# Optimization experiments

Measured on AMD Instinct MI355X. Metric: run time of the kernel, lower is better.

The kernel has to match this reference:

```python
import jax, jax.numpy as jnp
import numpy as np

# Adaptive-LIF constants (Yin et al. spiking RNN, which this thesis repo builds on)
B_J0 = 0.01    # baseline threshold
BETA = 1.8     # adaptation strength
GAMMA = 0.5    # surrogate gradient scale
LENS = 0.5     # surrogate gaussian width
HIGHT = 0.15   # multi-gaussian side-lobe height
SCALE = 6.0    # side-lobe width multiplier


def _gaussian(x, mu, sigma):
    return jnp.exp(-((x - mu) ** 2) / (2.0 * sigma ** 2)) / (jnp.sqrt(2.0 * jnp.pi) * sigma)


@jax.custom_vjp
def spike_fn(v):
    # Heaviside spike with multi-gaussian surrogate gradient
    return (v > 0).astype(v.dtype)

def _spike_fwd(v):
    return spike_fn(v), v

def _spike_bwd(v, g):
    sg = (_gaussian(v, 0.0, LENS) * (1.0 + HIGHT)
          - _gaussian(v, LENS, SCALE * LENS) * HIGHT
          - _gaussian(v, -LENS, SCALE * LENS) * HIGHT)
    return (g * sg * GAMMA,)

spike_fn.defvjp(_spike_fwd, _spike_bwd)


def setup_inputs() -> dict:
    key = jax.random.key(0)
    ks = jax.random.split(key, 16)
    B, S, C, H, O = 256, 250, 700, 256, 20

    def lin(k, fan_in, shape):  # nn.Linear default init
        lim = 1.0 / np.sqrt(fan_in)
        return jax.random.uniform(k, shape, jnp.float32, -lim, lim)

    def tau(k, mean, std, shape):
        return jnp.clip(mean + std * jax.random.normal(k, shape, jnp.float32), 1.0, None)

    return {
        "x": jax.random.normal(ks[0], (B, S, C), jnp.float32),
        # forward spiking cell (tauM ~ N(20, ~5), tauAdp ~ N(200, ~50))
        "W_in_f": lin(ks[1], C, (C, H)), "b_in_f": lin(ks[2], C, (H,)),
        "W_rec_f": lin(ks[3], H, (H, H)), "b_rec_f": lin(ks[4], H, (H,)),
        "tau_m_f": tau(ks[5], 20.0, 5.0, (H,)),
        "tau_adp_f": tau(ks[6], 200.0, 50.0, (H,)),
        # backward spiking cell
        "W_in_b": lin(ks[7], C, (C, H)), "b_in_b": lin(ks[8], C, (H,)),
        "W_rec_b": lin(ks[9], H, (H, H)), "b_rec_b": lin(ks[10], H, (H,)),
        "tau_m_b": tau(ks[11], 20.0, 5.0, (H,)),
        "tau_adp_b": tau(ks[12], 200.0, 50.0, (H,)),
        # readout leaky integrator over concat(fw, bw) = 512 -> 20, tauM ~ N(3, 1)
        "W_out": lin(ks[13], 2 * H, (2 * H, O)), "b_out": lin(ks[14], 2 * H, (O,)),
        "tau_m_out": tau(ks[15], 3.0, 1.0, (O,)),
    }


def reference(x, W_in_f, b_in_f, W_rec_f, b_rec_f, tau_m_f, tau_adp_f,
              W_in_b, b_in_b, W_rec_b, b_rec_b, tau_m_b, tau_adp_b,
              W_out, b_out, tau_m_out):
    B, S, C = x.shape
    H = W_in_f.shape[1]
    O = W_out.shape[1]

    alpha_f = jnp.exp(-1.0 / tau_m_f); ro_f = jnp.exp(-1.0 / tau_adp_f)
    alpha_b = jnp.exp(-1.0 / tau_m_b); ro_b = jnp.exp(-1.0 / tau_adp_b)
    alpha_o = jnp.exp(-1.0 / tau_m_out)

    # Batch the feed-forward input projections over all timesteps: [S, B, H]
    proj_f = jnp.einsum("bsc,ch->sbh", x, W_in_f) + b_in_f
    proj_b = jnp.einsum("bsc,ch->sbh", x[:, ::-1], W_in_b) + b_in_b

    def cell(in_t, mem, spk, bb, W_rec, b_rec, alpha, ro):
        # mem_update_adp: adaptive threshold LIF
        d = in_t + spk @ W_rec + b_rec
        bb = ro * bb + (1.0 - ro) * spk
        thr = B_J0 + BETA * bb
        mem = mem * alpha + (1.0 - alpha) * d - thr * spk
        spk = spike_fn(mem - thr)
        return mem, spk, bb

    def step(carry, xs):
        mem_f, spk_f, bb_f, mem_b, spk_b, bb_b, mem_o = carry
        in_f, in_b = xs
        mem_f, spk_f, bb_f = cell(in_f, mem_f, spk_f, bb_f, W_rec_f, b_rec_f, alpha_f, ro_f)
        mem_b, spk_b, bb_b = cell(in_b, mem_b, spk_b, bb_b, W_rec_b, b_rec_b, alpha_b, ro_b)
        # readout integrator over concat(fw, bw) spikes (method=1 integrates every step)
        merged = jnp.concatenate([spk_f, spk_b], axis=-1)
        mem_o = mem_o * alpha_o + (1.0 - alpha_o) * (merged @ W_out + b_out)
        return (mem_f, spk_f, bb_f, mem_b, spk_b, bb_b, mem_o), None

    z = jnp.zeros((B, H), x.dtype)
    b0 = jnp.full((B, H), B_J0, x.dtype)
    carry0 = (z, z, b0, z, z, b0, jnp.zeros((B, O), x.dtype))
    carry, _ = jax.lax.scan(step, carry0, (proj_f, proj_b))
    return jax.nn.log_softmax(carry[-1], axis=-1)
```

## Files before the change

kernel.cpp:

```cpp
#include <hip/hip_runtime.h>
#include <cstdint>
#include <cstddef>

#define S_LEN 250
#define BATCH 256
#define CIN   700
#define HID   256
#define OUT_N 20
#define KSTEPS 22

typedef __attribute__((ext_vector_type(8))) short bf16x8;
typedef __attribute__((ext_vector_type(4))) float f32x4;

__device__ __forceinline__ ushort f2bf_rne(float f) {
    uint u = __float_as_uint(f);
    uint r = (u + 0x7FFFu + ((u >> 16) & 1u)) >> 16;
    return (ushort)r;
}
__device__ __forceinline__ float bf2f(ushort h) {
    return __uint_as_float(((uint)h) << 16);
}

__global__ __launch_bounds__(256) void proj_mfma(
    const float* __restrict__ x,
    const float* __restrict__ Wf, const float* __restrict__ Wb,
    const float* __restrict__ biasf, const float* __restrict__ biasb,
    float* __restrict__ P)
{
    __shared__ ushort AsH[128][40];
    __shared__ ushort AsL[128][40];
    __shared__ ushort BsH[256][40];
    __shared__ ushort BsL[256][40];

    const int nt = blockIdx.x;
    const int mt = blockIdx.y;
    const int m0 = mt * 128;
    const float* W   = nt ? Wb : Wf;
    const float* bia = nt ? biasb : biasf;

    const int tid  = threadIdx.x;
    const int lane = tid & 63;
    const int wv   = tid >> 6;
    const int wr   = wv >> 1;
    const int wc   = wv & 1;
    const int l15  = lane & 15;
    const int l4   = lane >> 4;

    const int as  = tid & 7;
    const int arr = tid >> 3;

    f32x4 acc[4][8];
#pragma unroll
    for (int i = 0; i < 4; i++)
#pragma unroll
        for (int j = 0; j < 8; j++)
            acc[i][j] = (f32x4){0.f, 0.f, 0.f, 0.f};

    float4 av[4];
    float bv[32];

#define PROJ_LOAD(K0_) do {                                                   \
        const int ka_ = (K0_) + as * 4;                                       \
        const bool aok_ = (ka_ + 3) < CIN;                                    \
        _Pragma("unroll")                                                     \
        for (int i_ = 0; i_ < 4; i_++) {                                      \
            av[i_] = make_float4(0.f, 0.f, 0.f, 0.f);                         \
            if (aok_)                                                         \
                av[i_] = *(const float4*)&x[(size_t)(m0 + arr + 32 * i_) * CIN + ka_]; \
        }                                                                     \
        _Pragma("unroll")                                                     \
        for (int j_ = 0; j_ < 32; j_++) {                                     \
            const int kb_ = (K0_) + j_;                                       \
            bv[j_] = (kb_ < CIN) ? W[(size_t)kb_ * HID + tid] : 0.f;          \
        }                                                                     \
    } while (0)

#define PROJ_CVT_WRITE() do {                                                 \
        _Pragma("unroll")                                                     \
        for (int i_ = 0; i_ < 4; i_++) {                                      \
            const int row_ = arr + 32 * i_;                                   \
            ushort4 h_, l_;                                                   \
            h_.x = f2bf_rne(av[i_].x); l_.x = f2bf_rne(__fsub_rn(av[i_].x, bf2f(h_.x))); \
            h_.y = f2bf_rne(av[i_].y); l_.y = f2bf_rne(__fsub_rn(av[i_].y, bf2f(h_.y))); \
            h_.z = f2bf_rne(av[i_].z); l_.z = f2bf_rne(__fsub_rn(av[i_].z, bf2f(h_.z))); \
            h_.w = f2bf_rne(av[i_].w); l_.w = f2bf_rne(__fsub_rn(av[i_].w, bf2f(h_.w))); \
            *(ushort4*)&AsH[row_][as * 4] = h_;                               \
            *(ushort4*)&AsL[row_][as * 4] = l_;                               \
        }                                                                     \
        _Pragma("unroll")                                                     \
        for (int q_ = 0; q_ < 8; q_++) {                                      \
            ushort4 h_, l_;                                                   \
            float v0_ = bv[q_ * 4 + 0], v1_ = bv[q_ * 4 + 1];                 \
            float v2_ = bv[q_ * 4 + 2], v3_ = bv[q_ * 4 + 3];                 \
            h_.x = f2bf_rne(v0_); l_.x = f2bf_rne(__fsub_rn(v0_, bf2f(h_.x))); \
            h_.y = f2bf_rne(v1_); l_.y = f2bf_rne(__fsub_rn(v1_, bf2f(h_.y))); \
            h_.z = f2bf_rne(v2_); l_.z = f2bf_rne(__fsub_rn(v2_, bf2f(h_.z))); \
            h_.w = f2bf_rne(v3_); l_.w = f2bf_rne(__fsub_rn(v3_, bf2f(h_.w))); \
            *(ushort4*)&BsH[tid][q_ * 4] = h_;                               \
            *(ushort4*)&BsL[tid][q_ * 4] = l_;                               \
        }                                                                     \
    } while (0)

    PROJ_LOAD(0);
    PROJ_CVT_WRITE();

    for (int kt = 0; kt < KSTEPS; kt++) {
        __syncthreads();
        if (kt + 1 < KSTEPS)
            PROJ_LOAD((kt + 1) * 32);

#pragma unroll
        for (int fc = 0; fc < 8; fc++) {
            const bf16x8 bHf = *(const bf16x8*)&BsH[wc * 128 + fc * 16 + l15][l4 * 8];
            const bf16x8 bLf = *(const bf16x8*)&BsL[wc * 128 + fc * 16 + l15][l4 * 8];
#pragma unroll
            for (int fr = 0; fr < 4; fr++) {
                const bf16x8 aHf = *(const bf16x8*)&AsH[wr * 64 + fr * 16 + l15][l4 * 8];
                const bf16x8 aLf = *(const bf16x8*)&AsL[wr * 64 + fr * 16 + l15][l4 * 8];
                acc[fr][fc] = __builtin_amdgcn_mfma_f32_16x16x32_bf16(
                    aHf, bHf, acc[fr][fc], 0, 0, 0);
                acc[fr][fc] = __builtin_amdgcn_mfma_f32_16x16x32_bf16(
                    aHf, bLf, acc[fr][fc], 0, 0, 0);
                acc[fr][fc] = __builtin_amdgcn_mfma_f32_16x16x32_bf16(
                    aLf, bHf, acc[fr][fc], 0, 0, 0);
            }
        }

        __syncthreads();
        if (kt + 1 < KSTEPS)
            PROJ_CVT_WRITE();
    }

#undef PROJ_LOAD
#undef PROJ_CVT_WRITE

#pragma unroll
    for (int fc = 0; fc < 8; fc++) {
        const int col = wc * 128 + fc * 16 + l15;
        const float bvs = bia[col];
#pragma unroll
        for (int fr = 0; fr < 4; fr++) {
#pragma unroll
            for (int j = 0; j < 4; j++) {
                const int row = m0 + wr * 64 + fr * 16 + l4 * 4 + j;
                P[(size_t)row * 512 + nt * HID + col] =
                    __fadd_rn(acc[fr][fc][j], bvs);
            }
        }
    }
}

__global__ __launch_bounds__(512, 2) void scan_mfma(
    const float* __restrict__ P,
    const float* __restrict__ Wrecf, const float* __restrict__ brecf,
    const float* __restrict__ taumf, const float* __restrict__ tauaf,
    const float* __restrict__ Wrecb, const float* __restrict__ brecb,
    const float* __restrict__ taumb, const float* __restrict__ tauab,
    const float* __restrict__ Wout, const float* __restrict__ taumo,
    float* __restrict__ Pst)
{
    const int g  = blockIdx.x;
    const int d  = blockIdx.y;
    const int b0 = g * 16;
    const bool fw = (d == 0);

    const int tid  = threadIdx.x;
    const int lane = tid & 63;
    const int w    = tid >> 6;
    const int l15  = lane & 15;
    const int l4   = lane >> 4;

    __shared__ ushort Sp[2][16][264];

    {
        ushort* p = &Sp[0][0][0];
        for (int i = tid; i < 2 * 16 * 264; i += 512) p[i] = 0;
    }

    const float* Wrec = fw ? Wrecf : Wrecb;

    bf16x8 whf[8][2], wlf[8][2];
#pragma unroll
    for (int kt = 0; kt < 8; kt++)
#pragma unroll
        for (int ct = 0; ct < 2; ct++) {
            const int c = w * 32 + ct * 16 + l15;
#pragma unroll
            for (int j = 0; j < 8; j++) {
                const float v = Wrec[(size_t)(kt * 32 + l4 * 8 + j) * HID + c];
                const ushort h = f2bf_rne(v);
                const ushort l = f2bf_rne(__fsub_rn(v, bf2f(h)));
                whf[kt][ct][j] = (short)h;
                wlf[kt][ct][j] = (short)l;
            }
        }

    bf16x8 woh[2], wol[2];
#pragma unroll
    for (int t = 0; t < 2; t++) {
        const int o = t * 16 + l15;
#pragma unroll
        for (int j = 0; j < 8; j++) {
            float v = 0.f;
            if (o < OUT_N)
                v = Wout[(size_t)(d * HID + w * 32 + l4 * 8 + j) * OUT_N + o];
            const ushort h = f2bf_rne(v);
            const ushort l = f2bf_rne(__fsub_rn(v, bf2f(h)));
            woh[t][j] = (short)h;
            wol[t][j] = (short)l;
        }
    }

    float alpha_[2], ro_[2], omA_[2], omR_[2], brc_[2];
#pragma unroll
    for (int t = 0; t < 2; t++) {
        const int c = w * 32 + t * 16 + l15;
        alpha_[t] = expf(__fdiv_rn(-1.f, fw ? taumf[c] : taumb[c]));
        ro_[t]    = expf(__fdiv_rn(-1.f, fw ? tauaf[c] : tauab[c]));
        omA_[t]   = __fsub_rn(1.f, alpha_[t]);
        omR_[t]   = __fsub_rn(1.f, ro_[t]);
        brc_[t]   = fw ? brecf[c] : brecb[c];
    }
    float ao_[2], omo_[2];
#pragma unroll
    for (int t = 0; t < 2; t++) {
        const int o = t * 16 + l15;
        if (o < OUT_N) {
            ao_[t]  = expf(__fdiv_rn(-1.f, taumo[o]));
            omo_[t] = __fsub_rn(1.f, ao_[t]);
        } else { ao_[t] = 0.f; omo_[t] = 0.f; }
    }

    float mem[2][4], bbv[2][4], spkv[2][4], z[2][4];
#pragma unroll
    for (int t = 0; t < 2; t++)
#pragma unroll
        for (int j = 0; j < 4; j++) {
            mem[t][j] = 0.f; bbv[t][j] = 0.01f; spkv[t][j] = 0.f; z[t][j] = 0.f;
        }

    float pv[2][4];
    {
        const int srow = fw ? 0 : (S_LEN - 1);
#pragma unroll
        for (int t = 0; t < 2; t++)
#pragma unroll
            for (int j = 0; j < 4; j++)
                pv[t][j] = P[((size_t)(b0 + l4 * 4 + j) * S_LEN + srow) * 512
                             + d * HID + w * 32 + t * 16 + l15];
    }

    for (int s = 0; s < S_LEN; s++) {
        const int cur = s & 1, prev = cur ^ 1;

        float pv_next[2][4];
        {
            const int sn   = (s + 1 < S_LEN) ? s + 1 : S_LEN - 1;
            const int srow = fw ? sn : (S_LEN - 1 - sn);
#pragma unroll
            for (int t = 0; t < 2; t++)
#pragma unroll
                for (int j = 0; j < 4; j++)
                    pv_next[t][j] = P[((size_t)(b0 + l4 * 4 + j) * S_LEN + srow) * 512
                                      + d * HID + w * 32 + t * 16 + l15];
        }

        __syncthreads();

        f32x4 acc[2];
        acc[0] = (f32x4){0.f, 0.f, 0.f, 0.f};
        acc[1] = (f32x4){0.f, 0.f, 0.f, 0.f};
#pragma unroll
        for (int kt = 0; kt < 8; kt++) {
            const bf16x8 a = *(const bf16x8*)&Sp[prev][l15][kt * 32 + l4 * 8];
            acc[0] = __builtin_amdgcn_mfma_f32_16x16x32_bf16(a, whf[kt][0], acc[0], 0, 0, 0);
            acc[0] = __builtin_amdgcn_mfma_f32_16x16x32_bf16(a, wlf[kt][0], acc[0], 0, 0, 0);
            acc[1] = __builtin_amdgcn_mfma_f32_16x16x32_bf16(a, whf[kt][1], acc[1], 0, 0, 0);
            acc[1] = __builtin_amdgcn_mfma_f32_16x16x32_bf16(a, wlf[kt][1], acc[1], 0, 0, 0);
        }

#pragma unroll
        for (int t = 0; t < 2; t++) {
#pragma unroll
            for (int j = 0; j < 4; j++) {
                const float dd = __fadd_rn(__fadd_rn(pv[t][j], acc[t][j]), brc_[t]);
                bbv[t][j] = __fadd_rn(__fmul_rn(ro_[t], bbv[t][j]),
                                      __fmul_rn(omR_[t], spkv[t][j]));
                const float thr = __fadd_rn(0.01f, __fmul_rn(1.8f, bbv[t][j]));
                mem[t][j] = __fsub_rn(
                    __fadd_rn(__fmul_rn(mem[t][j], alpha_[t]),
                              __fmul_rn(omA_[t], dd)),
                    __fmul_rn(thr, spkv[t][j]));
                const bool sp = __fsub_rn(mem[t][j], thr) > 0.f;
                spkv[t][j] = sp ? 1.f : 0.f;
                Sp[cur][l4 * 4 + j][w * 32 + t * 16 + l15] =
                    sp ? (ushort)0x3F80 : (ushort)0;
            }
        }

        asm volatile("s_waitcnt lgkmcnt(0)" ::: "memory");
        __builtin_amdgcn_sched_barrier(0);

        {
            const bf16x8 ar = *(const bf16x8*)&Sp[cur][l15][w * 32 + l4 * 8];
            f32x4 S0 = (f32x4){0.f, 0.f, 0.f, 0.f};
            f32x4 S1 = (f32x4){0.f, 0.f, 0.f, 0.f};
            S0 = __builtin_amdgcn_mfma_f32_16x16x32_bf16(ar, woh[0], S0, 0, 0, 0);
            S0 = __builtin_amdgcn_mfma_f32_16x16x32_bf16(ar, wol[0], S0, 0, 0, 0);
            S1 = __builtin_amdgcn_mfma_f32_16x16x32_bf16(ar, woh[1], S1, 0, 0, 0);
            S1 = __builtin_amdgcn_mfma_f32_16x16x32_bf16(ar, wol[1], S1, 0, 0, 0);
#pragma unroll
            for (int j = 0; j < 4; j++) {
                z[0][j] = __fmaf_rn(ao_[0], z[0][j], __fmul_rn(omo_[0], S0[j]));
                z[1][j] = __fmaf_rn(ao_[1], z[1][j], __fmul_rn(omo_[1], S1[j]));
            }
        }

#pragma unroll
        for (int t = 0; t < 2; t++)
#pragma unroll
            for (int j = 0; j < 4; j++) pv[t][j] = pv_next[t][j];
    }

    __syncthreads();

    float* stash = Pst + ((size_t)b0 * S_LEN) * 512 + d * HID;
#pragma unroll
    for (int j = 0; j < 4; j++) {
        const int r = l4 * 4 + j;
        const int idx0 = w * 320 + r * 16 + l15;
        stash[(size_t)(idx0 >> 8) * 512 + (idx0 & 255)] = z[0][j];
        if (l15 < 4) {
            const int idx1 = w * 320 + 256 + r * 4 + l15;
            stash[(size_t)(idx1 >> 8) * 512 + (idx1 & 255)] = z[1][j];
        }
    }
}

__global__ __launch_bounds__(64) void merge_out(
    const float* __restrict__ Pst, const float* __restrict__ bout,
    const float* __restrict__ taumo, float* __restrict__ out)
{
    const int bb = blockIdx.x;
    const int o  = threadIdx.x;
    const int g  = bb >> 4, r = bb & 15;

    float val = 0.f, v = -3.0e38f;
    if (o < OUT_N) {
        float tot = 0.f;
#pragma unroll
        for (int d2 = 0; d2 < 2; d2++) {
            const float* stash = Pst + ((size_t)(g * 16) * S_LEN) * 512 + d2 * HID;
#pragma unroll
            for (int w2 = 0; w2 < 8; w2++) {
                const int idx = (o < 16) ? (w2 * 320 + r * 16 + o)
                                         : (w2 * 320 + 256 + r * 4 + (o - 16));
                tot = __fadd_rn(tot, stash[(size_t)(idx >> 8) * 512 + (idx & 255)]);
            }
        }
        const float aS = expf(__fdiv_rn(-(float)S_LEN, taumo[o]));
        val = __fadd_rn(tot, __fmul_rn(bout[o], __fsub_rn(1.f, aS)));
        v = val;
    }
    float mx = v;
#pragma unroll
    for (int d2 = 1; d2 < 64; d2 <<= 1)
        mx = fmaxf(mx, __shfl_xor(mx, d2, 64));
    float e = (o < OUT_N) ? expf(__fsub_rn(val, mx)) : 0.f;
#pragma unroll
    for (int d2 = 1; d2 < 64; d2 <<= 1)
        e += __shfl_xor(e, d2, 64);
    if (o < OUT_N)
        out[(size_t)bb * OUT_N + o] =
            __fsub_rn(__fsub_rn(val, mx), logf(e));
}

extern "C" void kernel_launch(void* const* d_in, const int* in_sizes, int n_in,
                              void* d_out, int out_size, void* d_ws, size_t ws_size,
                              hipStream_t stream) {
    const float* x         = (const float*)d_in[0];
    const float* W_in_f    = (const float*)d_in[1];
    const float* b_in_f    = (const float*)d_in[2];
    const float* W_rec_f   = (const float*)d_in[3];
    const float* b_rec_f   = (const float*)d_in[4];
    const float* tau_m_f   = (const float*)d_in[5];
    const float* tau_adp_f = (const float*)d_in[6];
    const float* W_in_b    = (const float*)d_in[7];
    const float* b_in_b    = (const float*)d_in[8];
    const float* W_rec_b   = (const float*)d_in[9];
    const float* b_rec_b   = (const float*)d_in[10];
    const float* tau_m_b   = (const float*)d_in[11];
    const float* tau_adp_b = (const float*)d_in[12];
    const float* W_out     = (const float*)d_in[13];
    const float* b_out     = (const float*)d_in[14];
    const float* tau_m_o   = (const float*)d_in[15];
    float* out = (float*)d_out;
    float* P   = (float*)d_ws;

    proj_mfma<<<dim3(2, 500), dim3(256), 0, stream>>>(
        x, W_in_f, W_in_b, b_in_f, b_in_b, P);
    scan_mfma<<<dim3(16, 2), dim3(512), 0, stream>>>(
        P, W_rec_f, b_rec_f, tau_m_f, tau_adp_f,
        W_rec_b, b_rec_b, tau_m_b, tau_adp_b,
        W_out, tau_m_o, P);
    merge_out<<<dim3(BATCH), dim3(64), 0, stream>>>(
        P, b_out, tau_m_o, out);
}
```

Before: 455.0 us.

## Split scan across 16 waves with half of recurrent weights staged in LDS

The recurrent scan now uses 1024 threads (16 waves), each wave owning 16 hidden columns instead of 32. This halves the per-wave serial MFMA chain and elementwise work. Half of the bf16 hi/lo split of W_rec stays in registers and the other half is held in shared memory, because the registers cannot hold all of it at this wave count. The readout MFMA is moved to run on the previous step's spikes, so one lgkmcnt wait and one sched barrier per step go away, with a final readout added after the loop. The costs are extra LDS traffic for the weight reads and larger per-block LDS usage.

```diff
diff --git a/kernel.cpp b/kernel.cpp
--- a/kernel.cpp
+++ b/kernel.cpp
@@ -150,7 +150,7 @@
     }
 }
 
-__global__ __launch_bounds__(512, 2) void scan_mfma(
+__global__ __launch_bounds__(1024, 4) void scan_mfma16(
     const float* __restrict__ P,
     const float* __restrict__ Wrecf, const float* __restrict__ brecf,
     const float* __restrict__ taumf, const float* __restrict__ tauaf,
@@ -169,140 +169,136 @@
     const int w    = tid >> 6;
     const int l15  = lane & 15;
     const int l4   = lane >> 4;
+    const int c    = w * 16 + l15;
 
     __shared__ ushort Sp[2][16][264];
+    __shared__ ushort WH[256][132];
+    __shared__ ushort WL[256][132];
 
     {
         ushort* p = &Sp[0][0][0];
-        for (int i = tid; i < 2 * 16 * 264; i += 512) p[i] = 0;
+        for (int i = tid; i < 2 * 16 * 264; i += 1024) p[i] = 0;
     }
 
     const float* Wrec = fw ? Wrecf : Wrecb;
 
-    bf16x8 whf[8][2], wlf[8][2];
-#pragma unroll
-    for (int kt = 0; kt < 8; kt++)
-#pragma unroll
-        for (int ct = 0; ct < 2; ct++) {
-            const int c = w * 32 + ct * 16 + l15;
+    {
+        const int cc = tid & 255;
+        const int kq = tid >> 8;
+        for (int k2 = 0; k2 < 32; k2++) {
+            const int k = 128 + kq * 32 + k2;
+            const float v = Wrec[(size_t)k * HID + cc];
+            const ushort h = f2bf_rne(v);
+            const ushort l = f2bf_rne(__fsub_rn(v, bf2f(h)));
+            WH[cc][k - 128] = h;
+            WL[cc][k - 128] = l;
+        }
+    }
+
+    bf16x8 whf[4], wlf[4];
+#pragma unroll
+    for (int kt = 0; kt < 4; kt++) {
+#pragma unroll
+        for (int j = 0; j < 8; j++) {
+            const float v = Wrec[(size_t)(kt * 32 + l4 * 8 + j) * HID + c];
+            const ushort h = f2bf_rne(v);
+            const ushort l = f2bf_rne(__fsub_rn(v, bf2f(h)));
+            whf[kt][j] = (short)h;
+            wlf[kt][j] = (short)l;
+        }
+    }
+
+    bf16x8 woh[2], wol[2];
+#pragma unroll
+    for (int t = 0; t < 2; t++)
+#pragma unroll
+        for (int j = 0; j < 8; j++) { woh[t][j] = 0; wol[t][j] = 0; }
+    if (!(w & 1)) {
+#pragma unroll
+        for (int t = 0; t < 2; t++) {
+            const int o = t * 16 + l15;
 #pragma unroll
             for (int j = 0; j < 8; j++) {
-                const float v = Wrec[(size_t)(kt * 32 + l4 * 8 + j) * HID + c];
+                float v = 0.f;
+                if (o < OUT_N)
+                    v = Wout[(size_t)(d * HID + w * 16 + l4 * 8 + j) * OUT_N + o];
                 const ushort h = f2bf_rne(v);
                 const ushort l = f2bf_rne(__fsub_rn(v, bf2f(h)));
-                whf[kt][ct][j] = (short)h;
-                wlf[kt][ct][j] = (short)l;
-            }
-        }
-
-    bf16x8 woh[2], wol[2];
-#pragma unroll
-    for (int t = 0; t < 2; t++) {
-        const int o = t * 16 + l15;
-#pragma unroll
-        for (int j = 0; j < 8; j++) {
-            float v = 0.f;
-            if (o < OUT_N)
-                v = Wout[(size_t)(d * HID + w * 32 + l4 * 8 + j) * OUT_N + o];
-            const ushort h = f2bf_rne(v);
-            const ushort l = f2bf_rne(__fsub_rn(v, bf2f(h)));
-            woh[t][j] = (short)h;
-            wol[t][j] = (short)l;
-        }
-    }
-
-    float alpha_[2], ro_[2], omA_[2], omR_[2], brc_[2];
-#pragma unroll
-    for (int t = 0; t < 2; t++) {
-        const int c = w * 32 + t * 16 + l15;
-        alpha_[t] = expf(__fdiv_rn(-1.f, fw ? taumf[c] : taumb[c]));
-        ro_[t]    = expf(__fdiv_rn(-1.f, fw ? tauaf[c] : tauab[c]));
-        omA_[t]   = __fsub_rn(1.f, alpha_[t]);
-        omR_[t]   = __fsub_rn(1.f, ro_[t]);
-        brc_[t]   = fw ? brecf[c] : brecb[c];
-    }
-    float ao_[2], omo_[2];
-#pragma unroll
-    for (int t = 0; t < 2; t++) {
-        const int o = t * 16 + l15;
-        if (o < OUT_N) {
-            ao_[t]  = expf(__fdiv_rn(-1.f, taumo[o]));
-            omo_[t] = __fsub_rn(1.f, ao_[t]);
-        } else { ao_[t] = 0.f; omo_[t] = 0.f; }
-    }
-
-    float mem[2][4], bbv[2][4], spkv[2][4], z[2][4];
-#pragma unroll
-    for (int t = 0; t < 2; t++)
-#pragma unroll
-        for (int j = 0; j < 4; j++) {
-            mem[t][j] = 0.f; bbv[t][j] = 0.01f; spkv[t][j] = 0.f; z[t][j] = 0.f;
-        }
-
-    float pv[2][4];
+                woh[t][j] = (short)h;
+                wol[t][j] = (short)l;
+            }
+        }
+    }
+
+    const float alpha = expf(__fdiv_rn(-1.f, fw ? taumf[c] : taumb[c]));
+    const float ro    = expf(__fdiv_rn(-1.f, fw ? tauaf[c] : tauab[c]));
+    const float omA   = __fsub_rn(1.f, alpha);
+    const float omR   = __fsub_rn(1.f, ro);
+    const float brc   = fw ? brecf[c] : brecb[c];
+
+    float ao_[2] = {0.f, 0.f}, omo_[2] = {0.f, 0.f};
+    if (!(w & 1)) {
+#pragma unroll
+        for (int t = 0; t < 2; t++) {
+            const int o = t * 16 + l15;
+            if (o < OUT_N) {
+                ao_[t]  = expf(__fdiv_rn(-1.f, taumo[o]));
+                omo_[t] = __fsub_rn(1.f, ao_[t]);
+            }
+        }
+    }
+
+    float mem[4], bbv[4], spkv[4], z[2][4];
+#pragma unroll
+    for (int j = 0; j < 4; j++) {
+        mem[j] = 0.f; bbv[j] = 0.01f; spkv[j] = 0.f;
+        z[0][j] = 0.f; z[1][j] = 0.f;
+    }
+
+    float pv[4];
     {
         const int srow = fw ? 0 : (S_LEN - 1);
 #pragma unroll
-        for (int t = 0; t < 2; t++)
-#pragma unroll
-            for (int j = 0; j < 4; j++)
-                pv[t][j] = P[((size_t)(b0 + l4 * 4 + j) * S_LEN + srow) * 512
-                             + d * HID + w * 32 + t * 16 + l15];
-    }
+        for (int j = 0; j < 4; j++)
+            pv[j] = P[((size_t)(b0 + l4 * 4 + j) * S_LEN + srow) * 512
+                      + d * HID + c];
+    }
+
+    __syncthreads();
 
     for (int s = 0; s < S_LEN; s++) {
         const int cur = s & 1, prev = cur ^ 1;
 
-        float pv_next[2][4];
+        float pv_next[4];
         {
             const int sn   = (s + 1 < S_LEN) ? s + 1 : S_LEN - 1;
             const int srow = fw ? sn : (S_LEN - 1 - sn);
 #pragma unroll
-            for (int t = 0; t < 2; t++)
-#pragma unroll
-                for (int j = 0; j < 4; j++)
-                    pv_next[t][j] = P[((size_t)(b0 + l4 * 4 + j) * S_LEN + srow) * 512
-                                      + d * HID + w * 32 + t * 16 + l15];
+            for (int j = 0; j < 4; j++)
+                pv_next[j] = P[((size_t)(b0 + l4 * 4 + j) * S_LEN + srow) * 512
+                               + d * HID + c];
         }
 
         __syncthreads();
 
-        f32x4 acc[2];
-        acc[0] = (f32x4){0.f, 0.f, 0.f, 0.f};
-        acc[1] = (f32x4){0.f, 0.f, 0.f, 0.f};
-#pragma unroll
-        for (int kt = 0; kt < 8; kt++) {
+        f32x4 acc = (f32x4){0.f, 0.f, 0.f, 0.f};
+#pragma unroll
+        for (int kt = 0; kt < 4; kt++) {
             const bf16x8 a = *(const bf16x8*)&Sp[prev][l15][kt * 32 + l4 * 8];
-            acc[0] = __builtin_amdgcn_mfma_f32_16x16x32_bf16(a, whf[kt][0], acc[0], 0, 0, 0);
-            acc[0] = __builtin_amdgcn_mfma_f32_16x16x32_bf16(a, wlf[kt][0], acc[0], 0, 0, 0);
-            acc[1] = __builtin_amdgcn_mfma_f32_16x16x32_bf16(a, whf[kt][1], acc[1], 0, 0, 0);
-            acc[1] = __builtin_amdgcn_mfma_f32_16x16x32_bf16(a, wlf[kt][1], acc[1], 0, 0, 0);
-        }
-
-#pragma unroll
-        for (int t = 0; t < 2; t++) {
-#pragma unroll
-            for (int j = 0; j < 4; j++) {
-                const float dd = __fadd_rn(__fadd_rn(pv[t][j], acc[t][j]), brc_[t]);
-                bbv[t][j] = __fadd_rn(__fmul_rn(ro_[t], bbv[t][j]),
-                                      __fmul_rn(omR_[t], spkv[t][j]));
-                const float thr = __fadd_rn(0.01f, __fmul_rn(1.8f, bbv[t][j]));
-                mem[t][j] = __fsub_rn(
-                    __fadd_rn(__fmul_rn(mem[t][j], alpha_[t]),
-                              __fmul_rn(omA_[t], dd)),
-                    __fmul_rn(thr, spkv[t][j]));
-                const bool sp = __fsub_rn(mem[t][j], thr) > 0.f;
-                spkv[t][j] = sp ? 1.f : 0.f;
-                Sp[cur][l4 * 4 + j][w * 32 + t * 16 + l15] =
-                    sp ? (ushort)0x3F80 : (ushort)0;
-            }
-        }
-
-        asm volatile("s_waitcnt lgkmcnt(0)" ::: "memory");
-        __builtin_amdgcn_sched_barrier(0);
-
-        {
-            const bf16x8 ar = *(const bf16x8*)&Sp[cur][l15][w * 32 + l4 * 8];
+            acc = __builtin_amdgcn_mfma_f32_16x16x32_bf16(a, whf[kt], acc, 0, 0, 0);
+            acc = __builtin_amdgcn_mfma_f32_16x16x32_bf16(a, wlf[kt], acc, 0, 0, 0);
+        }
+#pragma unroll
+        for (int kt = 4; kt < 8; kt++) {
+            const bf16x8 a  = *(const bf16x8*)&Sp[prev][l15][kt * 32 + l4 * 8];
+            const bf16x8 bh = *(const bf16x8*)&WH[c][(kt - 4) * 32 + l4 * 8];
+            const bf16x8 bl = *(const bf16x8*)&WL[c][(kt - 4) * 32 + l4 * 8];
+            acc = __builtin_amdgcn_mfma_f32_16x16x32_bf16(a, bh, acc, 0, 0, 0);
+            acc = __builtin_amdgcn_mfma_f32_16x16x32_bf16(a, bl, acc, 0, 0, 0);
+        }
+
+        if (!(w & 1)) {
+            const bf16x8 ar = *(const bf16x8*)&Sp[prev][l15][w * 16 + l4 * 8];
             f32x4 S0 = (f32x4){0.f, 0.f, 0.f, 0.f};
             f32x4 S1 = (f32x4){0.f, 0.f, 0.f, 0.f};
             S0 = __builtin_amdgcn_mfma_f32_16x16x32_bf16(ar, woh[0], S0, 0, 0, 0);
@@ -317,22 +313,50 @@
         }
 
 #pragma unroll
-        for (int t = 0; t < 2; t++)
-#pragma unroll
-            for (int j = 0; j < 4; j++) pv[t][j] = pv_next[t][j];
+        for (int j = 0; j < 4; j++) {
+            const float dd = __fadd_rn(__fadd_rn(pv[j], acc[j]), brc);
+            bbv[j] = __fadd_rn(__fmul_rn(ro, bbv[j]),
+                               __fmul_rn(omR, spkv[j]));
+            const float thr = __fadd_rn(0.01f, __fmul_rn(1.8f, bbv[j]));
+            mem[j] = __fsub_rn(
+                __fadd_rn(__fmul_rn(mem[j], alpha), __fmul_rn(omA, dd)),
+                __fmul_rn(thr, spkv[j]));
+            const bool sp = __fsub_rn(mem[j], thr) > 0.f;
+            spkv[j] = sp ? 1.f : 0.f;
+            Sp[cur][l4 * 4 + j][c] = sp ? (ushort)0x3F80 : (ushort)0;
+        }
+
+#pragma unroll
+        for (int j = 0; j < 4; j++) pv[j] = pv_next[j];
     }
 
     __syncthreads();
 
-    float* stash = Pst + ((size_t)b0 * S_LEN) * 512 + d * HID;
-#pragma unroll
-    for (int j = 0; j < 4; j++) {
-        const int r = l4 * 4 + j;
-        const int idx0 = w * 320 + r * 16 + l15;
-        stash[(size_t)(idx0 >> 8) * 512 + (idx0 & 255)] = z[0][j];
-        if (l15 < 4) {
-            const int idx1 = w * 320 + 256 + r * 4 + l15;
-            stash[(size_t)(idx1 >> 8) * 512 + (idx1 & 255)] = z[1][j];
+    if (!(w & 1)) {
+        const bf16x8 ar = *(const bf16x8*)&Sp[1][l15][w * 16 + l4 * 8];
+        f32x4 S0 = (f32x4){0.f, 0.f, 0.f, 0.f};
+        f32x4 S1 = (f32x4){0.f, 0.f, 0.f, 0.f};
+        S0 = __builtin_amdgcn_mfma_f32_16x16x32_bf16(ar, woh[0], S0, 0, 0, 0);
+        S0 = __builtin_amdgcn_mfma_f32_16x16x32_bf16(ar, wol[0], S0, 0, 0, 0);
+        S1 = __builtin_amdgcn_mfma_f32_16x16x32_bf16(ar, woh[1], S1, 0, 0, 0);
+        S1 = __builtin_amdgcn_mfma_f32_16x16x32_bf16(ar, wol[1], S1, 0, 0, 0);
+#pragma unroll
+        for (int j = 0; j < 4; j++) {
+            z[0][j] = __fmaf_rn(ao_[0], z[0][j], __fmul_rn(omo_[0], S0[j]));
+            z[1][j] = __fmaf_rn(ao_[1], z[1][j], __fmul_rn(omo_[1], S1[j]));
+        }
+
+        float* stash = Pst + ((size_t)b0 * S_LEN) * 512 + d * HID;
+        const int ws = w >> 1;
+#pragma unroll
+        for (int j = 0; j < 4; j++) {
+            const int r = l4 * 4 + j;
+            const int idx0 = ws * 320 + r * 16 + l15;
+            stash[(size_t)(idx0 >> 8) * 512 + (idx0 & 255)] = z[0][j];
+            if (l15 < 4) {
+                const int idx1 = ws * 320 + 256 + r * 4 + l15;
+                stash[(size_t)(idx1 >> 8) * 512 + (idx1 & 255)] = z[1][j];
+            }
         }
     }
 }
@@ -399,7 +423,7 @@
 
     proj_mfma<<<dim3(2, 500), dim3(256), 0, stream>>>(
         x, W_in_f, W_in_b, b_in_f, b_in_b, P);
-    scan_mfma<<<dim3(16, 2), dim3(512), 0, stream>>>(
+    scan_mfma16<<<dim3(16, 2), dim3(1024), 0, stream>>>(
         P, W_rec_f, b_rec_f, tau_m_f, tau_adp_f,
         W_rec_b, b_rec_b, tau_m_b, tau_adp_b,
         W_out, tau_m_o, P);
```

New measurement: 511.2 us. 12.3% more time.

## Use int8 MFMA with split hi/lo quantized recurrent weights for spike matmul

Applied to the files above, without the earlier changes.

Replaces the bf16 hi/lo split recurrent matmul with int8 MFMA (16x16x64). The recurrent weights are quantized per column to a 16-bit fixed-point value split into two int8 halves, and the binary spikes go into a new int8 shared buffer. This halves the MFMA instruction count per step and reduces register use for the weights. In exchange it adds a per-column max scan at setup and an extra shared-memory store per spike, and it changes numerical precision to about 1/16000 of the column max, which could flip spikes near the threshold.

```diff
diff --git a/kernel.cpp b/kernel.cpp
--- a/kernel.cpp
+++ b/kernel.cpp
@@ -11,6 +11,7 @@
 
 typedef __attribute__((ext_vector_type(8))) short bf16x8;
 typedef __attribute__((ext_vector_type(4))) float f32x4;
+typedef __attribute__((ext_vector_type(4))) int   i32x4;
 
 __device__ __forceinline__ ushort f2bf_rne(float f) {
     uint u = __float_as_uint(f);
@@ -171,29 +172,51 @@
     const int l4   = lane >> 4;
 
     __shared__ ushort Sp[2][16][264];
+    __shared__ signed char Sp8[2][16][272];
 
     {
         ushort* p = &Sp[0][0][0];
         for (int i = tid; i < 2 * 16 * 264; i += 512) p[i] = 0;
+        signed char* p8 = &Sp8[0][0][0];
+        for (int i = tid; i < 2 * 16 * 272; i += 512) p8[i] = 0;
     }
 
     const float* Wrec = fw ? Wrecf : Wrecb;
 
-    bf16x8 whf[8][2], wlf[8][2];
-#pragma unroll
-    for (int kt = 0; kt < 8; kt++)
-#pragma unroll
-        for (int ct = 0; ct < 2; ct++) {
-            const int c = w * 32 + ct * 16 + l15;
-#pragma unroll
-            for (int j = 0; j < 8; j++) {
-                const float v = Wrec[(size_t)(kt * 32 + l4 * 8 + j) * HID + c];
-                const ushort h = f2bf_rne(v);
-                const ushort l = f2bf_rne(__fsub_rn(v, bf2f(h)));
-                whf[kt][ct][j] = (short)h;
-                wlf[kt][ct][j] = (short)l;
-            }
-        }
+    float s2_[2];
+    i32x4 b8h[2][4], b8l[2][4];
+#pragma unroll
+    for (int t = 0; t < 2; t++) {
+        const int c = w * 32 + t * 16 + l15;
+        float cmax = 0.f;
+        for (int k = 0; k < HID; k++)
+            cmax = fmaxf(cmax, fabsf(Wrec[(size_t)k * HID + c]));
+        cmax = fmaxf(cmax, 1e-30f);
+        const float s2  = __fdiv_rn(cmax, 16000.f);
+        const float inv = __fdiv_rn(16000.f, cmax);
+        s2_[t] = s2;
+#pragma unroll
+        for (int kt = 0; kt < 4; kt++) {
+            int hw[4], lw[4];
+#pragma unroll
+            for (int wd = 0; wd < 4; wd++) {
+                int hb = 0, lb = 0;
+#pragma unroll
+                for (int byt = 0; byt < 4; byt++) {
+                    const int k = kt * 64 + l4 * 16 + wd * 4 + byt;
+                    const float v = Wrec[(size_t)k * HID + c];
+                    const int q  = (int)lrintf(__fmul_rn(v, inv));
+                    const int hi = (q + 128) >> 8;
+                    const int lo = q - (hi << 8);
+                    hb |= (hi & 255) << (8 * byt);
+                    lb |= (lo & 255) << (8 * byt);
+                }
+                hw[wd] = hb; lw[wd] = lb;
+            }
+            b8h[t][kt] = (i32x4){hw[0], hw[1], hw[2], hw[3]};
+            b8l[t][kt] = (i32x4){lw[0], lw[1], lw[2], lw[3]};
+        }
+    }
 
     bf16x8 woh[2], wol[2];
 #pragma unroll
@@ -267,23 +290,25 @@
 
         __syncthreads();
 
-        f32x4 acc[2];
-        acc[0] = (f32x4){0.f, 0.f, 0.f, 0.f};
-        acc[1] = (f32x4){0.f, 0.f, 0.f, 0.f};
-#pragma unroll
-        for (int kt = 0; kt < 8; kt++) {
-            const bf16x8 a = *(const bf16x8*)&Sp[prev][l15][kt * 32 + l4 * 8];
-            acc[0] = __builtin_amdgcn_mfma_f32_16x16x32_bf16(a, whf[kt][0], acc[0], 0, 0, 0);
-            acc[0] = __builtin_amdgcn_mfma_f32_16x16x32_bf16(a, wlf[kt][0], acc[0], 0, 0, 0);
-            acc[1] = __builtin_amdgcn_mfma_f32_16x16x32_bf16(a, whf[kt][1], acc[1], 0, 0, 0);
-            acc[1] = __builtin_amdgcn_mfma_f32_16x16x32_bf16(a, wlf[kt][1], acc[1], 0, 0, 0);
+        i32x4 accH0 = (i32x4){0, 0, 0, 0}, accL0 = (i32x4){0, 0, 0, 0};
+        i32x4 accH1 = (i32x4){0, 0, 0, 0}, accL1 = (i32x4){0, 0, 0, 0};
+#pragma unroll
+        for (int kt = 0; kt < 4; kt++) {
+            const i32x4 a8 = *(const i32x4*)&Sp8[prev][l15][kt * 64 + l4 * 16];
+            accH0 = __builtin_amdgcn_mfma_i32_16x16x64_i8(a8, b8h[0][kt], accH0, 0, 0, 0);
+            accL0 = __builtin_amdgcn_mfma_i32_16x16x64_i8(a8, b8l[0][kt], accL0, 0, 0, 0);
+            accH1 = __builtin_amdgcn_mfma_i32_16x16x64_i8(a8, b8h[1][kt], accH1, 0, 0, 0);
+            accL1 = __builtin_amdgcn_mfma_i32_16x16x64_i8(a8, b8l[1][kt], accL1, 0, 0, 0);
         }
 
 #pragma unroll
         for (int t = 0; t < 2; t++) {
 #pragma unroll
             for (int j = 0; j < 4; j++) {
-                const float dd = __fadd_rn(__fadd_rn(pv[t][j], acc[t][j]), brc_[t]);
+                const int th = t ? accH1[j] : accH0[j];
+                const int tl = t ? accL1[j] : accL0[j];
+                const float accv = __fmul_rn(s2_[t], (float)(th * 256 + tl));
+                const float dd = __fadd_rn(__fadd_rn(pv[t][j], accv), brc_[t]);
                 bbv[t][j] = __fadd_rn(__fmul_rn(ro_[t], bbv[t][j]),
                                       __fmul_rn(omR_[t], spkv[t][j]));
                 const float thr = __fadd_rn(0.01f, __fmul_rn(1.8f, bbv[t][j]));
@@ -293,8 +318,10 @@
                     __fmul_rn(thr, spkv[t][j]));
                 const bool sp = __fsub_rn(mem[t][j], thr) > 0.f;
                 spkv[t][j] = sp ? 1.f : 0.f;
-                Sp[cur][l4 * 4 + j][w * 32 + t * 16 + l15] =
-                    sp ? (ushort)0x3F80 : (ushort)0;
+                const int row = l4 * 4 + j;
+                const int col = w * 32 + t * 16 + l15;
+                Sp[cur][row][col]  = sp ? (ushort)0x3F80 : (ushort)0;
+                Sp8[cur][row][col] = sp ? (signed char)1 : (signed char)0;
             }
         }
 
```

After: 510.0 us. +12.1%, slower.
